# Kernel tuning notes

Measured on AMD Instinct MI355X. Metric: run time of the kernel, lower is better.

## Reference

```python
import jax, jax.numpy as jnp
import numpy as np

B, T, D, H, E, K = 8, 4096, 768, 3072, 4, 2


def setup_inputs() -> dict:
    key = jax.random.key(0)
    ks = jax.random.split(key, 7)
    s = 0.02
    return {
        "x": jax.random.normal(ks[0], (B, T, D), dtype=jnp.float32),
        "router_w": jax.random.normal(ks[1], (D, E), dtype=jnp.float32) * s,
        "router_b": jnp.zeros((E,), dtype=jnp.float32),
        "W1": jax.random.normal(ks[2], (E, D, H), dtype=jnp.float32) * s,
        "b1": jnp.zeros((E, H), dtype=jnp.float32),
        "W2": jax.random.normal(ks[3], (E, H, D), dtype=jnp.float32) * s,
        "b2": jnp.zeros((E, D), dtype=jnp.float32),
    }


def reference(x, router_w, router_b, W1, b1, W2, b2):
    # Router: softmax over experts, then top-k selection.
    logits = jnp.einsum('btd,de->bte', x, router_w) + router_b        # [B,T,E]
    probs = jax.nn.softmax(logits, axis=-1)                           # [B,T,E]
    topk_probs, topk_idx = jax.lax.top_k(probs, K)                    # [B,T,K]

    # Per-expert combine weight: sum of top-k probs assigned to expert e.
    onehot = jax.nn.one_hot(topk_idx, E, dtype=x.dtype)               # [B,T,K,E]
    w = jnp.einsum('btk,btke->bte', topk_probs, onehot)               # [B,T,E]

    # Expert FFNs (exact-erf GELU matches torch F.gelu default).
    out = jnp.zeros_like(x)
    for e in range(E):
        h = jax.nn.gelu(jnp.einsum('btd,dh->bth', x, W1[e]) + b1[e], approximate=False)
        y = jnp.einsum('bth,hd->btd', h, W2[e]) + b2[e]
        out = out + w[..., e:e + 1] * y

    # Load-balance loss: expert assignment counts (non-differentiable, from int idx).
    counts = onehot.sum(axis=(0, 1, 2))                               # [E]
    token_fraction = counts / counts.sum()
    router_prob_mean = probs.mean(axis=(0, 1))                        # [E]
    load_balance_loss = E * jnp.sum(router_prob_mean * token_fraction)
    return out, load_balance_loss
```

## Files before the change

### kernel.cpp

```cpp
#include <hip/hip_runtime.h>
#include <hip/hip_bf16.h>
#include <hip/hip_fp16.h>

#define N_TOK 32768
#define D_DIM 768
#define H_DIM 3072
#define E_NUM 4
#define MT_PAD (N_TOK + 512)

#define TILE_E 4096

typedef _Float16 f16_t;
typedef _Float16 f16x8 __attribute__((ext_vector_type(8)));
typedef float f32x4 __attribute__((ext_vector_type(4)));

__device__ __forceinline__ f16_t f2h(float f) { return (f16_t)f; }

__device__ __forceinline__ void gload16(const void* g, void* l) {
  __builtin_amdgcn_global_load_lds(
      (const __attribute__((address_space(1))) void*)g,
      (__attribute__((address_space(3))) void*)l,
      16, 0, 0);
}

__device__ __forceinline__ int xcd_swizzle(int f, int nwg) {
  const int q = nwg >> 3, r = nwg & 7;
  const int xcd = f & 7, pos = f >> 3;
  return (xcd < r ? xcd * (q + 1) : r * (q + 1) + (xcd - r) * q) + pos;
}


__global__ __launch_bounds__(256) void fill_kernel(unsigned* __restrict__ idx0,
                                                   unsigned* __restrict__ idx1) {
  const int t = blockIdx.x * 256 + threadIdx.x;
  for (int i = t; i < MT_PAD; i += gridDim.x * 256) {
    idx0[i] = 0xFFFFFFFFu;
    idx1[i] = 0xFFFFFFFFu;
  }
}

__global__ __launch_bounds__(256) void transform_kernel(
    const float* __restrict__ in, f16_t* __restrict__ outT,
    int R, int C, int NT, int KT) {
  __shared__ float tile[32][33];
  const int ez = blockIdx.z;
  in += (size_t)ez * R * C;
  const int c0 = blockIdx.x * 32, r0 = blockIdx.y * 32;
  const int tc = threadIdx.x & 31, tr = threadIdx.x >> 5;
#pragma unroll
  for (int i = 0; i < 32; i += 8)
    tile[tr + i][tc] = in[(size_t)(r0 + tr + i) * C + c0 + tc];
  __syncthreads();
  const int kt = r0 >> 5, g = tc >> 3, kk = tc & 7;
#pragma unroll
  for (int i = 0; i < 32; i += 8) {
    const int n = c0 + tr + i;
    const int nt = n >> 7, rl = n & 127;
    outT[(((size_t)(ez * NT + nt)) * KT + kt) * TILE_E + g * 1024 + rl * 8 + kk]
        = f2h(tile[tc][tr + i]);
  }
}

__global__ __launch_bounds__(256) void router_kernel(
    const float* __restrict__ x, const float* __restrict__ rw, const float* __restrict__ rb,
    float* __restrict__ wcomb, int* __restrict__ pairinfo,
    float* __restrict__ psum_part, int* __restrict__ cnt_part,
    int* __restrict__ cnt0_part, int* __restrict__ cnt1_part) {
  __shared__ float rwT[E_NUM][D_DIM];
  __shared__ float prW[4][E_NUM];
  __shared__ int   cnW[4][E_NUM];
  __shared__ int   cn0W[4][E_NUM];
  __shared__ int   cn1W[4][E_NUM];
  const int tid = threadIdx.x;
  for (int i = tid; i < D_DIM * E_NUM; i += 256) {
    int k = i >> 2, e = i & 3;
    rwT[e][k] = rw[i];
  }
  __syncthreads();
  const int lane = tid & 63, wv_ = tid >> 6;
  float pacc[E_NUM] = {0.f, 0.f, 0.f, 0.f};
  int   cacc[E_NUM] = {0, 0, 0, 0};
  int   c0acc[E_NUM] = {0, 0, 0, 0};
  int   c1acc[E_NUM] = {0, 0, 0, 0};
  const int tok0 = blockIdx.x * 32 + wv_ * 8;
  for (int t = 0; t < 8; ++t) {
    const int m = tok0 + t;
    const float* xr = x + (size_t)m * D_DIM;
    float s0 = 0.f, s1 = 0.f, s2 = 0.f, s3 = 0.f;
#pragma unroll
    for (int i = 0; i < D_DIM / 64; ++i) {
      int k = lane + i * 64;
      float xv = xr[k];
      s0 += xv * rwT[0][k]; s1 += xv * rwT[1][k];
      s2 += xv * rwT[2][k]; s3 += xv * rwT[3][k];
    }
#pragma unroll
    for (int off = 32; off >= 1; off >>= 1) {
      s0 += __shfl_xor(s0, off); s1 += __shfl_xor(s1, off);
      s2 += __shfl_xor(s2, off); s3 += __shfl_xor(s3, off);
    }
    if (lane == 0) {
      float lg[4] = {s0 + rb[0], s1 + rb[1], s2 + rb[2], s3 + rb[3]};
      float mx = fmaxf(fmaxf(lg[0], lg[1]), fmaxf(lg[2], lg[3]));
      float p[4]; float den = 0.f;
#pragma unroll
      for (int e = 0; e < 4; ++e) { p[e] = expf(lg[e] - mx); den += p[e]; }
      float inv = 1.f / den;
#pragma unroll
      for (int e = 0; e < 4; ++e) p[e] *= inv;
      int i1 = 0;
#pragma unroll
      for (int e = 1; e < 4; ++e) if (p[e] > p[i1]) i1 = e;
      int i2 = (i1 == 0) ? 1 : 0;
#pragma unroll
      for (int e = 0; e < 4; ++e) if (e != i1 && p[e] > p[i2]) i2 = e;
      float4 wvout;
      wvout.x = (0 == i1 || 0 == i2) ? p[0] : 0.f;
      wvout.y = (1 == i1 || 1 == i2) ? p[1] : 0.f;
      wvout.z = (2 == i1 || 2 == i2) ? p[2] : 0.f;
      wvout.w = (3 == i1 || 3 == i2) ? p[3] : 0.f;
      ((float4*)wcomb)[m] = wvout;
      const int emin = (i1 < i2) ? i1 : i2;
      const int emax = (i1 < i2) ? i2 : i1;
      pairinfo[m] = emin | (emax << 4);
      c0acc[emin]++; c1acc[emax]++;
#pragma unroll
      for (int e = 0; e < 4; ++e) pacc[e] += p[e];
      cacc[i1]++; cacc[i2]++;
    }
  }
  if (lane == 0) {
#pragma unroll
    for (int e = 0; e < 4; ++e) {
      prW[wv_][e] = pacc[e]; cnW[wv_][e] = cacc[e];
      cn0W[wv_][e] = c0acc[e]; cn1W[wv_][e] = c1acc[e];
    }
  }
  __syncthreads();
  if (tid < 4) {
    float ps = prW[0][tid] + prW[1][tid] + prW[2][tid] + prW[3][tid];
    int   cs = cnW[0][tid] + cnW[1][tid] + cnW[2][tid] + cnW[3][tid];
    psum_part[blockIdx.x * 4 + tid] = ps;
    cnt_part[blockIdx.x * 4 + tid]  = cs;
    cnt0_part[blockIdx.x * 4 + tid] = cn0W[0][tid] + cn0W[1][tid] + cn0W[2][tid] + cn0W[3][tid];
    cnt1_part[blockIdx.x * 4 + tid] = cn1W[0][tid] + cn1W[1][tid] + cn1W[2][tid] + cn1W[3][tid];
  }
}

__global__ void loss_kernel(const float* __restrict__ psum_part,
                            const int* __restrict__ cnt_part,
                            float* __restrict__ loss_out, int nblk) {
  const int lane = threadIdx.x;
  float ps[4] = {0.f, 0.f, 0.f, 0.f};
  int   cs[4] = {0, 0, 0, 0};
  for (int r = lane; r < nblk; r += 64) {
#pragma unroll
    for (int e = 0; e < 4; ++e) { ps[e] += psum_part[r * 4 + e]; cs[e] += cnt_part[r * 4 + e]; }
  }
#pragma unroll
  for (int off = 32; off >= 1; off >>= 1) {
#pragma unroll
    for (int e = 0; e < 4; ++e) {
      ps[e] += __shfl_xor(ps[e], off);
      cs[e] += __shfl_xor(cs[e], off);
    }
  }
  if (lane == 0) {
    float loss = 0.f;
#pragma unroll
    for (int e = 0; e < 4; ++e) {
      float mean = ps[e] / (float)N_TOK;
      float frac = (float)cs[e] / (float)(N_TOK * 2);
      loss += mean * frac;
    }
    loss_out[0] = 4.f * loss;
  }
}

__global__ __launch_bounds__(256) void setup_kernel(const int* __restrict__ cnt0_part,
                                                    const int* __restrict__ cnt1_part,
                                                    int* __restrict__ meta, int nblk) {
  __shared__ int sh[8][32];
  const int ch = threadIdx.x >> 5, ln = threadIdx.x & 31;
  const int* src = (ch < 4) ? cnt0_part : cnt1_part;
  const int e = ch & 3;
  int s = 0;
  for (int b = ln; b < nblk; b += 32) s += src[b * 4 + e];
  sh[ch][ln] = s;
  __syncthreads();
  if (threadIdx.x == 0) {
    int c[8];
    for (int c2 = 0; c2 < 8; ++c2) {
      int t = 0;
      for (int l = 0; l < 32; ++l) t += sh[c2][l];
      c[c2] = t;
    }
    int pb = 0; meta[8] = 0;
    for (int e2 = 0; e2 < 4; ++e2) { pb += (c[e2] + 127) & ~127; meta[9 + e2] = pb; }
    pb = 0; meta[13] = 0;
    for (int e2 = 0; e2 < 4; ++e2) { pb += (c[4 + e2] + 127) & ~127; meta[14 + e2] = pb; }
    for (int e2 = 0; e2 < 4; ++e2) { meta[18 + e2] = meta[8 + e2]; meta[22 + e2] = meta[13 + e2]; }
  }
}

__global__ __launch_bounds__(256) void scatter_kernel(const int* __restrict__ pairinfo,
                                                      int* __restrict__ meta,
                                                      unsigned* __restrict__ idx0,
                                                      unsigned* __restrict__ idx1) {
  __shared__ int wcnt[2][4][4];
  __shared__ int blkbase[2][4];
  const int tid = threadIdx.x, lane = tid & 63, wv = tid >> 6;
  const int t = blockIdx.x * 256 + tid;
  const int info = pairinfo[t];
  const int esel0 = info & 15, esel1 = info >> 4;
  int rank0 = 0, rank1 = 0;
#pragma unroll
  for (int e = 0; e < 4; ++e) {
    unsigned long long m0 = __ballot(esel0 == e);
    if (esel0 == e) rank0 = __popcll(m0 & ((1ull << lane) - 1ull));
    unsigned long long m1 = __ballot(esel1 == e);
    if (esel1 == e) rank1 = __popcll(m1 & ((1ull << lane) - 1ull));
    if (lane == 0) { wcnt[0][wv][e] = __popcll(m0); wcnt[1][wv][e] = __popcll(m1); }
  }
  __syncthreads();
  int wbase0 = 0, wbase1 = 0;
  for (int w = 0; w < wv; ++w) { wbase0 += wcnt[0][w][esel0]; wbase1 += wcnt[1][w][esel1]; }
  if (tid < 8) {
    const int p = tid >> 2, e = tid & 3;
    const int tot = wcnt[p][0][e] + wcnt[p][1][e] + wcnt[p][2][e] + wcnt[p][3][e];
    blkbase[p][e] = atomicAdd(&meta[(p ? 22 : 18) + e], tot);
  }
  __syncthreads();
  idx0[blkbase[0][esel0] + wbase0 + rank0] = (unsigned)t;
  idx1[blkbase[1][esel1] + wbase1 + rank1] = (unsigned)t;
}

__global__ __launch_bounds__(256) void gather_kernel(
    const float* __restrict__ x, const unsigned* __restrict__ idx_p,
    f16_t* __restrict__ xg, int srow) {
  __shared__ unsigned idx_s[128];
  const int tid = threadIdx.x, mt = blockIdx.x;
  if (tid < 128) {
    const int gr = srow + mt * 128 + tid;
    idx_s[tid] = (gr < MT_PAD) ? idx_p[gr] : 0xFFFFFFFFu;
  }
  __syncthreads();
  f16_t* dst = xg + (size_t)mt * 24 * TILE_E;
  for (int i = tid; i < 128 * 96; i += 256) {
    const int r = i / 96, grp = i - r * 96;
    const unsigned v = idx_s[r];
    const float* src = x + (size_t)((v < N_TOK) ? v : 0u) * D_DIM + grp * 8;
    float4 f0 = ((const float4*)src)[0];
    float4 f1 = ((const float4*)src)[1];
    f16x8 h;
    h[0] = f2h(f0.x); h[1] = f2h(f0.y); h[2] = f2h(f0.z); h[3] = f2h(f0.w);
    h[4] = f2h(f1.x); h[5] = f2h(f1.y); h[6] = f2h(f1.z); h[7] = f2h(f1.w);
    const int kt = grp >> 2, g = grp & 3;
    *(f16x8*)&dst[(size_t)kt * TILE_E + g * 1024 + r * 8] = h;
  }
}

#define BM 128
#define BN 128

#define MFMA_HALF(AvBase, BvBase)                                                   \
  {                                                                                 \
    const f16x8* Av = (const f16x8*)(AvBase);                                       \
    const f16x8* Bv = (const f16x8*)(BvBase);                                       \
    const int gsel = (lane >> 4) * 128;                                             \
    f16x8 a[4], b[4];                                                               \
    _Pragma("unroll")                                                               \
    for (int mf = 0; mf < 4; ++mf) a[mf] = Av[gsel + wr * 64 + mf * 16 + (lane & 15)]; \
    _Pragma("unroll")                                                               \
    for (int nf = 0; nf < 4; ++nf) b[nf] = Bv[gsel + wc * 64 + nf * 16 + (lane & 15)]; \
    _Pragma("unroll")                                                               \
    for (int mf = 0; mf < 4; ++mf)                                                  \
      _Pragma("unroll")                                                             \
      for (int nf = 0; nf < 4; ++nf)                                                \
        acc[mf][nf] = __builtin_amdgcn_mfma_f32_16x16x32_f16(a[mf], b[nf], acc[mf][nf], 0, 0, 0); \
  }

__global__ __launch_bounds__(256, 3) void gemm1_kernel(
    const f16_t* __restrict__ xg, const f16_t* __restrict__ W1T,
    const float* __restrict__ b1, const int* __restrict__ pb_p,
    f16_t* __restrict__ HwP, int srow) {
  __shared__ __align__(16) f16_t As[2 * TILE_E];
  __shared__ __align__(16) f16_t Bs[2 * TILE_E];
  const int tid = threadIdx.x, lane = tid & 63, wid = tid >> 6;
  const int wg = xcd_swizzle(blockIdx.x, gridDim.x);
  const int ntile = wg % 24, mtile = wg / 24;
  const int m128 = srow + mtile * BM;
  if (m128 >= pb_p[4]) return;
  int e = 0;
  while (e < 3 && m128 >= pb_p[e + 1]) ++e;
  const int n0 = ntile * BN;

  const f16_t* abase = xg + (size_t)mtile * 24 * TILE_E + lane * 8;
  const f16_t* bbase = W1T + (size_t)(e * 24 + ntile) * 24 * TILE_E + lane * 8;

  auto stage = [&](int kt, int h) {
    const f16_t* a = abase + (size_t)kt * TILE_E;
    const f16_t* b = bbase + (size_t)kt * TILE_E;
    gload16(a + wid * 512,        &As[h * TILE_E + wid * 512]);
    gload16(a + 2048 + wid * 512, &As[h * TILE_E + 2048 + wid * 512]);
    gload16(b + wid * 512,        &Bs[h * TILE_E + wid * 512]);
    gload16(b + 2048 + wid * 512, &Bs[h * TILE_E + 2048 + wid * 512]);
  };

  const int wr = wid >> 1, wc = wid & 1;
  f32x4 acc[4][4] = {};

  float b1v[4];
#pragma unroll
  for (int nf = 0; nf < 4; ++nf)
    b1v[nf] = b1[e * H_DIM + n0 + wc * 64 + nf * 16 + (lane & 15)];

  const int NT2 = (D_DIM / 32) / 2;
  for (int t = 0; t < NT2; ++t) {
    stage(2 * t, 0);
    stage(2 * t + 1, 1);
    __syncthreads();
    MFMA_HALF(As, Bs);
    MFMA_HALF(As + TILE_E, Bs + TILE_E);
    __syncthreads();
  }

  const int colb = wc * 64 + (lane & 15);
#pragma unroll
  for (int mf = 0; mf < 4; ++mf) {
    const int rowb = wr * 64 + mf * 16 + ((lane >> 4) << 2);
#pragma unroll
    for (int nf = 0; nf < 4; ++nf) {
      const int col = n0 + colb + nf * 16;
      const int kt = col >> 5, g = (col >> 3) & 3, kk = col & 7;
#pragma unroll
      for (int j = 0; j < 4; ++j) {
        const int row = rowb + j;
        float v = acc[mf][nf][j] + b1v[nf];
        float gel = 0.5f * v * (1.0f + erff(v * 0.70710678118654752440f));
        HwP[((size_t)(mtile * 96 + kt)) * TILE_E + g * 1024 + row * 8 + kk] = f2h(gel);
      }
    }
  }
}

__global__ __launch_bounds__(256, 3) void gemm2_kernel(
    const f16_t* __restrict__ HwP, const f16_t* __restrict__ W2T,
    const float* __restrict__ b2, const float* __restrict__ wcomb,
    const unsigned* __restrict__ idx_p, const int* __restrict__ pb_p,
    float* __restrict__ out, int srow, int doAdd) {
  __shared__ __align__(16) f16_t As[2 * TILE_E];
  __shared__ __align__(16) f16_t Bs[2 * TILE_E];
  __shared__ unsigned idx_s[BM];
  __shared__ float w_s[BM];
  const int tid = threadIdx.x, lane = tid & 63, wid = tid >> 6;
  const int wg = xcd_swizzle(blockIdx.x, gridDim.x);
  const int ntile = wg % 6, mtile = wg / 6;
  const int m128 = srow + mtile * BM;
  if (m128 >= pb_p[4]) return;
  int e = 0;
  while (e < 3 && m128 >= pb_p[e + 1]) ++e;
  const int n0 = ntile * BN;

  if (tid < BM) idx_s[tid] = idx_p[m128 + tid];
  __syncthreads();
  if (tid < BM) {
    unsigned v = idx_s[tid];
    w_s[tid] = (v < N_TOK) ? wcomb[v * 4 + e] : 0.f;
  }

  const f16_t* abase = HwP + (size_t)mtile * 96 * TILE_E + lane * 8;
  const f16_t* bbase = W2T + (size_t)(e * 6 + ntile) * 96 * TILE_E + lane * 8;

  auto stage = [&](int kt, int h) {
    const f16_t* a = abase + (size_t)kt * TILE_E;
    const f16_t* b = bbase + (size_t)kt * TILE_E;
    gload16(a + wid * 512,        &As[h * TILE_E + wid * 512]);
    gload16(a + 2048 + wid * 512, &As[h * TILE_E + 2048 + wid * 512]);
    gload16(b + wid * 512,        &Bs[h * TILE_E + wid * 512]);
    gload16(b + 2048 + wid * 512, &Bs[h * TILE_E + 2048 + wid * 512]);
  };

  const int wr = wid >> 1, wc = wid & 1;
  f32x4 acc[4][4] = {};

  float b2v[4];
#pragma unroll
  for (int nf = 0; nf < 4; ++nf)
    b2v[nf] = b2[e * D_DIM + n0 + wc * 64 + nf * 16 + (lane & 15)];

  const int NT2 = (H_DIM / 32) / 2;
  for (int t = 0; t < NT2; ++t) {
    stage(2 * t, 0);
    stage(2 * t + 1, 1);
    __syncthreads();
    MFMA_HALF(As, Bs);
    MFMA_HALF(As + TILE_E, Bs + TILE_E);
    __syncthreads();
  }

  const int colb = wc * 64 + (lane & 15);
#pragma unroll
  for (int mf = 0; mf < 4; ++mf) {
    const int rowb = wr * 64 + mf * 16 + ((lane >> 4) << 2);
#pragma unroll
    for (int nf = 0; nf < 4; ++nf) {
      const int col = n0 + colb + nf * 16;
#pragma unroll
      for (int j = 0; j < 4; ++j) {
        const int row = rowb + j;
        const unsigned v = idx_s[row];
        if (v < N_TOK) {
          float contrib = w_s[row] * (acc[mf][nf][j] + b2v[nf]);
          float* po = out + (size_t)v * D_DIM + col;
          if (doAdd) *po += contrib; else *po = contrib;
        }
      }
    }
  }
}

extern "C" void kernel_launch(void* const* d_in, const int* in_sizes, int n_in,
                              void* d_out, int out_size, void* d_ws, size_t ws_size,
                              hipStream_t stream) {
  const float* x  = (const float*)d_in[0];
  const float* rw = (const float*)d_in[1];
  const float* rb = (const float*)d_in[2];
  const float* W1 = (const float*)d_in[3];
  const float* b1 = (const float*)d_in[4];
  const float* W2 = (const float*)d_in[5];
  const float* b2 = (const float*)d_in[6];
  float* out = (float*)d_out;

  char* ws = (char*)d_ws;
  size_t off = 0;
  auto alloc = [&](size_t bytes) -> void* {
    void* p = ws + off;
    off = (off + bytes + 255) & ~(size_t)255;
    return p;
  };
  f16_t* W1T = (f16_t*)alloc((size_t)E_NUM * D_DIM * H_DIM * sizeof(f16_t));
  f16_t* W2T = (f16_t*)alloc((size_t)E_NUM * D_DIM * H_DIM * sizeof(f16_t));
  float* wcomb = (float*)alloc((size_t)N_TOK * E_NUM * sizeof(float));
  float* psum_part = (float*)alloc((size_t)(N_TOK / 32) * 4 * sizeof(float));
  int*   cnt_part  = (int*)alloc((size_t)(N_TOK / 32) * 4 * sizeof(int));
  int*   cnt0_part = (int*)alloc((size_t)(N_TOK / 32) * 4 * sizeof(int));
  int*   cnt1_part = (int*)alloc((size_t)(N_TOK / 32) * 4 * sizeof(int));
  int*   pairinfo  = (int*)alloc((size_t)N_TOK * sizeof(int));
  int*   meta      = (int*)alloc(32 * sizeof(int));
  unsigned* idx0   = (unsigned*)alloc((size_t)MT_PAD * sizeof(unsigned));
  unsigned* idx1   = (unsigned*)alloc((size_t)MT_PAD * sizeof(unsigned));

  size_t avail = (ws_size > off) ? ws_size - off : 0;
  int hwrows = (int)(avail / 7680);
  if (hwrows > MT_PAD) hwrows = MT_PAD;
  hwrows &= ~127;
  if (hwrows < 128) hwrows = 128;
  const int chunks = (MT_PAD + hwrows - 1) / hwrows;
  f16_t* xg  = (f16_t*)(ws + off);
  f16_t* HwP = (f16_t*)(ws + off + (size_t)hwrows * D_DIM * sizeof(f16_t));

  const int nblk = N_TOK / 32;

  fill_kernel<<<128, 256, 0, stream>>>(idx0, idx1);
  transform_kernel<<<dim3(H_DIM / 32, D_DIM / 32, E_NUM), 256, 0, stream>>>(W1, W1T, D_DIM, H_DIM, 24, 24);
  transform_kernel<<<dim3(D_DIM / 32, H_DIM / 32, E_NUM), 256, 0, stream>>>(W2, W2T, H_DIM, D_DIM, 6, 96);
  router_kernel<<<nblk, 256, 0, stream>>>(x, rw, rb, wcomb, pairinfo,
                                          psum_part, cnt_part, cnt0_part, cnt1_part);
  loss_kernel<<<1, 64, 0, stream>>>(psum_part, cnt_part, out + (size_t)N_TOK * D_DIM, nblk);
  setup_kernel<<<1, 256, 0, stream>>>(cnt0_part, cnt1_part, meta, nblk);
  scatter_kernel<<<N_TOK / 256, 256, 0, stream>>>(pairinfo, meta, idx0, idx1);

  for (int pass = 0; pass < 2; ++pass) {
    const unsigned* ip = pass ? idx1 : idx0;
    const int* pbp = meta + (pass ? 13 : 8);
    for (int c = 0; c < chunks; ++c) {
      const int srow = c * hwrows;
      gather_kernel<<<hwrows / 128, 256, 0, stream>>>(x, ip, xg, srow);
      gemm1_kernel<<<(hwrows / 128) * 24, 256, 0, stream>>>(xg, W1T, b1, pbp, HwP, srow);
      gemm2_kernel<<<(hwrows / 128) * 6, 256, 0, stream>>>(HwP, W2T, b2, wcomb, ip, pbp, out, srow, pass);
    }
  }
}
```

Before: 1.000 ms.

## Triple-buffer gemm2 LDS tiles with async prefetch two stages ahead

Replaces gemm2's load-all-then-compute double-buffer loop with a three-slot LDS ring. Loads for tile t+2 are issued while tile t is being multiplied, with manual vmcnt waits and a single barrier per k-step. The aim is to overlap global-to-LDS transfers with MFMA work and drop one of the two syncthreads per iteration. In exchange it uses more LDS (48KB versus 32KB), which could reduce occupancy below the three blocks per CU set by launch_bounds. The hand-written waitcnt values must also exactly match the outstanding loads.

```diff
diff --git a/kernel.cpp b/kernel.cpp
--- a/kernel.cpp
+++ b/kernel.cpp
@@ -21,6 +21,14 @@
       (const __attribute__((address_space(1))) void*)g,
       (__attribute__((address_space(3))) void*)l,
       16, 0, 0);
+}
+
+__device__ __forceinline__ void pipe_barrier() {
+  asm volatile("" ::: "memory");
+  __builtin_amdgcn_sched_barrier(0);
+  __builtin_amdgcn_s_barrier();
+  __builtin_amdgcn_sched_barrier(0);
+  asm volatile("" ::: "memory");
 }
 
 __device__ __forceinline__ int xcd_swizzle(int f, int nwg) {
@@ -349,8 +357,8 @@
     const float* __restrict__ b2, const float* __restrict__ wcomb,
     const unsigned* __restrict__ idx_p, const int* __restrict__ pb_p,
     float* __restrict__ out, int srow, int doAdd) {
-  __shared__ __align__(16) f16_t As[2 * TILE_E];
-  __shared__ __align__(16) f16_t Bs[2 * TILE_E];
+  __shared__ __align__(16) f16_t As[3][TILE_E];
+  __shared__ __align__(16) f16_t Bs[3][TILE_E];
   __shared__ unsigned idx_s[BM];
   __shared__ float w_s[BM];
   const int tid = threadIdx.x, lane = tid & 63, wid = tid >> 6;
@@ -372,13 +380,13 @@
   const f16_t* abase = HwP + (size_t)mtile * 96 * TILE_E + lane * 8;
   const f16_t* bbase = W2T + (size_t)(e * 6 + ntile) * 96 * TILE_E + lane * 8;
 
-  auto stage = [&](int kt, int h) {
+  auto stage = [&](int kt, int buf) {
     const f16_t* a = abase + (size_t)kt * TILE_E;
     const f16_t* b = bbase + (size_t)kt * TILE_E;
-    gload16(a + wid * 512,        &As[h * TILE_E + wid * 512]);
-    gload16(a + 2048 + wid * 512, &As[h * TILE_E + 2048 + wid * 512]);
-    gload16(b + wid * 512,        &Bs[h * TILE_E + wid * 512]);
-    gload16(b + 2048 + wid * 512, &Bs[h * TILE_E + 2048 + wid * 512]);
+    gload16(a + wid * 512,        &As[buf][wid * 512]);
+    gload16(a + 2048 + wid * 512, &As[buf][2048 + wid * 512]);
+    gload16(b + wid * 512,        &Bs[buf][wid * 512]);
+    gload16(b + 2048 + wid * 512, &Bs[buf][2048 + wid * 512]);
   };
 
   const int wr = wid >> 1, wc = wid & 1;
@@ -389,14 +397,17 @@
   for (int nf = 0; nf < 4; ++nf)
     b2v[nf] = b2[e * D_DIM + n0 + wc * 64 + nf * 16 + (lane & 15)];
 
-  const int NT2 = (H_DIM / 32) / 2;
-  for (int t = 0; t < NT2; ++t) {
-    stage(2 * t, 0);
-    stage(2 * t + 1, 1);
-    __syncthreads();
-    MFMA_HALF(As, Bs);
-    MFMA_HALF(As + TILE_E, Bs + TILE_E);
-    __syncthreads();
+  stage(0, 0);
+  stage(1, 1);
+  const int NT = H_DIM / 32;
+  int cur = 0;
+  for (int t = 0; t < NT; ++t) {
+    if (t + 1 < NT) { asm volatile("s_waitcnt vmcnt(4)" ::: "memory"); }
+    else            { asm volatile("s_waitcnt vmcnt(0)" ::: "memory"); }
+    pipe_barrier();
+    if (t + 2 < NT) stage(t + 2, (t + 2) % 3);
+    MFMA_HALF(As[cur], Bs[cur]);
+    cur = (cur == 2) ? 0 : cur + 1;
   }
 
   const int colb = wc * 64 + (lane & 15);
```

Measured after the change: 1.235 ms. +23.5%, slower.

## Load A fragments directly to registers and remap waves to 4x1 layout

Applied to the files above, without the earlier changes.

Both GEMM kernels stop staging the A (activation) tile through LDS. Each wave now owns 32 rows by the full 128 columns and loads its A fragments straight from global memory into registers, and only the B (weight) tile is staged in shared memory. This halves LDS usage and the LDS read traffic for A, which may allow higher occupancy. In exchange, every wave reads all of B from LDS, doubling B reads per wave. The A loads are synchronous global loads issued right before the barrier, so their latency is exposed.

```diff
diff --git a/kernel.cpp b/kernel.cpp
--- a/kernel.cpp
+++ b/kernel.cpp
@@ -263,29 +263,26 @@
 #define BM 128
 #define BN 128
 
-#define MFMA_HALF(AvBase, BvBase)                                                   \
-  {                                                                                 \
-    const f16x8* Av = (const f16x8*)(AvBase);                                       \
-    const f16x8* Bv = (const f16x8*)(BvBase);                                       \
-    const int gsel = (lane >> 4) * 128;                                             \
-    f16x8 a[4], b[4];                                                               \
-    _Pragma("unroll")                                                               \
-    for (int mf = 0; mf < 4; ++mf) a[mf] = Av[gsel + wr * 64 + mf * 16 + (lane & 15)]; \
-    _Pragma("unroll")                                                               \
-    for (int nf = 0; nf < 4; ++nf) b[nf] = Bv[gsel + wc * 64 + nf * 16 + (lane & 15)]; \
-    _Pragma("unroll")                                                               \
-    for (int mf = 0; mf < 4; ++mf)                                                  \
-      _Pragma("unroll")                                                             \
-      for (int nf = 0; nf < 4; ++nf)                                                \
-        acc[mf][nf] = __builtin_amdgcn_mfma_f32_16x16x32_f16(a[mf], b[nf], acc[mf][nf], 0, 0, 0); \
+#define MFMA_H(a0_, a1_, BvBase)                                                     \
+  {                                                                                  \
+    const f16x8* Bv = (const f16x8*)(BvBase);                                        \
+    const int gsel = (lane >> 4) * 128;                                              \
+    f16x8 b[8];                                                                      \
+    _Pragma("unroll")                                                                \
+    for (int nf = 0; nf < 8; ++nf) b[nf] = Bv[gsel + nf * 16 + (lane & 15)];         \
+    _Pragma("unroll")                                                                \
+    for (int nf = 0; nf < 8; ++nf)                                                   \
+      acc[0][nf] = __builtin_amdgcn_mfma_f32_16x16x32_f16(a0_, b[nf], acc[0][nf], 0, 0, 0); \
+    _Pragma("unroll")                                                                \
+    for (int nf = 0; nf < 8; ++nf)                                                   \
+      acc[1][nf] = __builtin_amdgcn_mfma_f32_16x16x32_f16(a1_, b[nf], acc[1][nf], 0, 0, 0); \
   }
 
 __global__ __launch_bounds__(256, 3) void gemm1_kernel(
     const f16_t* __restrict__ xg, const f16_t* __restrict__ W1T,
     const float* __restrict__ b1, const int* __restrict__ pb_p,
     f16_t* __restrict__ HwP, int srow) {
-  __shared__ __align__(16) f16_t As[2 * TILE_E];
-  __shared__ __align__(16) f16_t Bs[2 * TILE_E];
+  __shared__ __align__(16) f16_t Bs[2][TILE_E];
   const int tid = threadIdx.x, lane = tid & 63, wid = tid >> 6;
   const int wg = xcd_swizzle(blockIdx.x, gridDim.x);
   const int ntile = wg % 24, mtile = wg / 24;
@@ -295,43 +292,47 @@
   while (e < 3 && m128 >= pb_p[e + 1]) ++e;
   const int n0 = ntile * BN;
 
-  const f16_t* abase = xg + (size_t)mtile * 24 * TILE_E + lane * 8;
+  const int wr = wid;
+  const f16_t* atile = xg + (size_t)mtile * 24 * TILE_E;
+  const int aoff0 = (lane >> 4) * 1024 + (wr * 32 + (lane & 15)) * 8;
+  const int aoff1 = aoff0 + 16 * 8;
   const f16_t* bbase = W1T + (size_t)(e * 24 + ntile) * 24 * TILE_E + lane * 8;
 
-  auto stage = [&](int kt, int h) {
-    const f16_t* a = abase + (size_t)kt * TILE_E;
+  auto stageB = [&](int kt, int h) {
     const f16_t* b = bbase + (size_t)kt * TILE_E;
-    gload16(a + wid * 512,        &As[h * TILE_E + wid * 512]);
-    gload16(a + 2048 + wid * 512, &As[h * TILE_E + 2048 + wid * 512]);
-    gload16(b + wid * 512,        &Bs[h * TILE_E + wid * 512]);
-    gload16(b + 2048 + wid * 512, &Bs[h * TILE_E + 2048 + wid * 512]);
+    gload16(b + wid * 512,        &Bs[h][wid * 512]);
+    gload16(b + 2048 + wid * 512, &Bs[h][2048 + wid * 512]);
   };
 
-  const int wr = wid >> 1, wc = wid & 1;
-  f32x4 acc[4][4] = {};
-
-  float b1v[4];
-#pragma unroll
-  for (int nf = 0; nf < 4; ++nf)
-    b1v[nf] = b1[e * H_DIM + n0 + wc * 64 + nf * 16 + (lane & 15)];
+  f32x4 acc[2][8] = {};
+
+  float b1v[8];
+#pragma unroll
+  for (int nf = 0; nf < 8; ++nf)
+    b1v[nf] = b1[e * H_DIM + n0 + nf * 16 + (lane & 15)];
 
   const int NT2 = (D_DIM / 32) / 2;
   for (int t = 0; t < NT2; ++t) {
-    stage(2 * t, 0);
-    stage(2 * t + 1, 1);
+    stageB(2 * t, 0);
+    stageB(2 * t + 1, 1);
+    const f16_t* a0t = atile + (size_t)(2 * t) * TILE_E;
+    const f16_t* a1t = atile + (size_t)(2 * t + 1) * TILE_E;
+    f16x8 a00 = *(const f16x8*)(a0t + aoff0);
+    f16x8 a01 = *(const f16x8*)(a0t + aoff1);
+    f16x8 a10 = *(const f16x8*)(a1t + aoff0);
+    f16x8 a11 = *(const f16x8*)(a1t + aoff1);
     __syncthreads();
-    MFMA_HALF(As, Bs);
-    MFMA_HALF(As + TILE_E, Bs + TILE_E);
+    MFMA_H(a00, a01, Bs[0]);
+    MFMA_H(a10, a11, Bs[1]);
     __syncthreads();
   }
 
-  const int colb = wc * 64 + (lane & 15);
-#pragma unroll
-  for (int mf = 0; mf < 4; ++mf) {
-    const int rowb = wr * 64 + mf * 16 + ((lane >> 4) << 2);
-#pragma unroll
-    for (int nf = 0; nf < 4; ++nf) {
-      const int col = n0 + colb + nf * 16;
+#pragma unroll
+  for (int mf = 0; mf < 2; ++mf) {
+    const int rowb = wr * 32 + mf * 16 + ((lane >> 4) << 2);
+#pragma unroll
+    for (int nf = 0; nf < 8; ++nf) {
+      const int col = n0 + nf * 16 + (lane & 15);
       const int kt = col >> 5, g = (col >> 3) & 3, kk = col & 7;
 #pragma unroll
       for (int j = 0; j < 4; ++j) {
@@ -349,8 +350,7 @@
     const float* __restrict__ b2, const float* __restrict__ wcomb,
     const unsigned* __restrict__ idx_p, const int* __restrict__ pb_p,
     float* __restrict__ out, int srow, int doAdd) {
-  __shared__ __align__(16) f16_t As[2 * TILE_E];
-  __shared__ __align__(16) f16_t Bs[2 * TILE_E];
+  __shared__ __align__(16) f16_t Bs[2][TILE_E];
   __shared__ unsigned idx_s[BM];
   __shared__ float w_s[BM];
   const int tid = threadIdx.x, lane = tid & 63, wid = tid >> 6;
@@ -369,43 +369,47 @@
     w_s[tid] = (v < N_TOK) ? wcomb[v * 4 + e] : 0.f;
   }
 
-  const f16_t* abase = HwP + (size_t)mtile * 96 * TILE_E + lane * 8;
+  const int wr = wid;
+  const f16_t* atile = HwP + (size_t)mtile * 96 * TILE_E;
+  const int aoff0 = (lane >> 4) * 1024 + (wr * 32 + (lane & 15)) * 8;
+  const int aoff1 = aoff0 + 16 * 8;
   const f16_t* bbase = W2T + (size_t)(e * 6 + ntile) * 96 * TILE_E + lane * 8;
 
-  auto stage = [&](int kt, int h) {
-    const f16_t* a = abase + (size_t)kt * TILE_E;
+  auto stageB = [&](int kt, int h) {
     const f16_t* b = bbase + (size_t)kt * TILE_E;
-    gload16(a + wid * 512,        &As[h * TILE_E + wid * 512]);
-    gload16(a + 2048 + wid * 512, &As[h * TILE_E + 2048 + wid * 512]);
-    gload16(b + wid * 512,        &Bs[h * TILE_E + wid * 512]);
-    gload16(b + 2048 + wid * 512, &Bs[h * TILE_E + 2048 + wid * 512]);
+    gload16(b + wid * 512,        &Bs[h][wid * 512]);
+    gload16(b + 2048 + wid * 512, &Bs[h][2048 + wid * 512]);
   };
 
-  const int wr = wid >> 1, wc = wid & 1;
-  f32x4 acc[4][4] = {};
-
-  float b2v[4];
-#pragma unroll
-  for (int nf = 0; nf < 4; ++nf)
-    b2v[nf] = b2[e * D_DIM + n0 + wc * 64 + nf * 16 + (lane & 15)];
+  f32x4 acc[2][8] = {};
+
+  float b2v[8];
+#pragma unroll
+  for (int nf = 0; nf < 8; ++nf)
+    b2v[nf] = b2[e * D_DIM + n0 + nf * 16 + (lane & 15)];
 
   const int NT2 = (H_DIM / 32) / 2;
   for (int t = 0; t < NT2; ++t) {
-    stage(2 * t, 0);
-    stage(2 * t + 1, 1);
+    stageB(2 * t, 0);
+    stageB(2 * t + 1, 1);
+    const f16_t* a0t = atile + (size_t)(2 * t) * TILE_E;
+    const f16_t* a1t = atile + (size_t)(2 * t + 1) * TILE_E;
+    f16x8 a00 = *(const f16x8*)(a0t + aoff0);
+    f16x8 a01 = *(const f16x8*)(a0t + aoff1);
+    f16x8 a10 = *(const f16x8*)(a1t + aoff0);
+    f16x8 a11 = *(const f16x8*)(a1t + aoff1);
     __syncthreads();
-    MFMA_HALF(As, Bs);
-    MFMA_HALF(As + TILE_E, Bs + TILE_E);
+    MFMA_H(a00, a01, Bs[0]);
+    MFMA_H(a10, a11, Bs[1]);
     __syncthreads();
   }
 
-  const int colb = wc * 64 + (lane & 15);
-#pragma unroll
-  for (int mf = 0; mf < 4; ++mf) {
-    const int rowb = wr * 64 + mf * 16 + ((lane >> 4) << 2);
-#pragma unroll
-    for (int nf = 0; nf < 4; ++nf) {
-      const int col = n0 + colb + nf * 16;
+#pragma unroll
+  for (int mf = 0; mf < 2; ++mf) {
+    const int rowb = wr * 32 + mf * 16 + ((lane >> 4) << 2);
+#pragma unroll
+    for (int nf = 0; nf < 8; ++nf) {
+      const int col = n0 + nf * 16 + (lane & 15);
 #pragma unroll
       for (int j = 0; j < 4; ++j) {
         const int row = rowb + j;
```

After: 1.120 ms. +12.0%, slower.
